# Kernel optimization log

Measured on AMD Instinct MI355X. Metric: run time of the kernel, lower is better.

The kernel has to match this reference:

```python
import jax, jax.numpy as jnp
import numpy as np

B, DIM, HEADS, HW = 32, 384, 8, 48
CH = DIM // HEADS  # 48 channels per head


def pool_matrix(H, s):
    # PyTorch AdaptiveAvgPool2d binning: start=floor(i*H/s), end=ceil((i+1)*H/s)
    P = np.zeros((s, H), np.float32)
    for i in range(s):
        a = (i * H) // s
        b = -((-(i + 1) * H) // s)
        P[i, a:b] = 1.0 / (b - a)
    return jnp.asarray(P)


def dwconv(x, w, b, p):
    # depthwise conv, NCHW, kernel [C,1,k,k], stride 1, symmetric pad p
    y = jax.lax.conv_general_dilated(
        x, w, (1, 1), [(p, p), (p, p)],
        dimension_numbers=('NCHW', 'OIHW', 'NCHW'),
        feature_group_count=x.shape[1])
    if b is not None:
        y = y + b[None, :, None, None]
    return y


def setup_inputs() -> dict:
    key = jax.random.key(0)
    ks = jax.random.split(key, 10)
    s = 0.02
    return {
        'x': jax.random.normal(ks[0], (B, DIM, HW, HW), jnp.float32),
        'ln_w': jnp.ones((DIM,), jnp.float32),
        'ln_b': jnp.zeros((DIM,), jnp.float32),
        'w_qkv': jax.random.normal(ks[1], (3 * DIM, DIM), jnp.float32) * s,
        'w_dw': jax.random.normal(ks[2], (3 * DIM, 1, 3, 3), jnp.float32) * s,
        'temperature': jnp.ones((HEADS, 1, 1), jnp.float32),
        'conv3_w': jax.random.normal(ks[3], (3 * CH, 1, 3, 3), jnp.float32) * s,
        'conv3_b': jnp.zeros((3 * CH,), jnp.float32),
        'conv5_w': jax.random.normal(ks[4], (3 * CH, 1, 5, 5), jnp.float32) * s,
        'conv5_b': jnp.zeros((3 * CH,), jnp.float32),
        'conv7_w': jax.random.normal(ks[5], (2 * CH, 1, 7, 7), jnp.float32) * s,
        'conv7_b': jnp.zeros((2 * CH,), jnp.float32),
        'w_proj': jax.random.normal(ks[6], (DIM, DIM), jnp.float32) * s,
    }


def reference(x, ln_w, ln_b, w_qkv, w_dw, temperature,
              conv3_w, conv3_b, conv5_w, conv5_b, conv7_w, conv7_b, w_proj):
    b, C, H, W = x.shape
    heads, Ch = HEADS, C // HEADS
    N = H * W
    # WithBias LayerNorm over channel dim (biased variance, eps 1e-5)
    mu = x.mean(axis=1, keepdims=True)
    var = ((x - mu) ** 2).mean(axis=1, keepdims=True)
    xn = (x - mu) / jnp.sqrt(var + 1e-5) * ln_w[None, :, None, None] + ln_b[None, :, None, None]
    # qkv: 1x1 conv then depthwise 3x3 (groups = 3*dim)
    qkv = jnp.einsum('bchw,oc->bohw', xn, w_qkv)
    qkv = dwconv(qkv, w_dw, None, 1)
    q, k, v = jnp.split(qkv, 3, axis=1)
    q = q.reshape(b, heads, Ch, N)
    k = k.reshape(b, heads, Ch, N)
    v = v.reshape(b, heads, Ch, N)
    # L2-normalize along token dim (F.normalize eps=1e-12)
    qn = q / jnp.maximum(jnp.linalg.norm(q, axis=-1, keepdims=True), 1e-12)
    kn = k / jnp.maximum(jnp.linalg.norm(k, axis=-1, keepdims=True), 1e-12)
    # channel attention [b,h,Ch,Ch]
    attn = jax.nn.relu(jnp.einsum('bhcn,bhdn->bhcd', qn, kn) * temperature[None])
    # ---- FilterModule (crpe) ----
    v_img = v.reshape(b, heads * Ch, H, W)
    # low-pass: 4 equal channel chunks, adaptive avg pool to (1,3,5,7), bilinear up
    chunk = (heads * Ch) // 4
    lp_parts = []
    for idx, sz in enumerate((1, 3, 5, 7)):
        part = v_img[:, idx * chunk:(idx + 1) * chunk]
        Pr = pool_matrix(H, sz)
        Pc = pool_matrix(W, sz)
        pooled = jnp.einsum('ph,bchw,qw->bcpq', Pr, part, Pc)
        lp_parts.append(jax.image.resize(pooled, (b, chunk, H, W), method='linear'))
    LP = jax.nn.relu(jnp.concatenate(lp_parts, axis=1))
    # high-pass: grouped depthwise convs on [3Ch, 3Ch, 2Ch] channel splits
    s0, s1 = 3 * Ch, 3 * Ch
    HP = jnp.concatenate([
        dwconv(v_img[:, :s0], conv3_w, conv3_b, 1),
        dwconv(v_img[:, s0:s0 + s1], conv5_w, conv5_b, 2),
        dwconv(v_img[:, s0 + s1:], conv7_w, conv7_b, 3),
    ], axis=1)
    HP = HP.reshape(b, heads, Ch, N)
    LPf = LP.reshape(b, heads, Ch, N)
    crpe = qn * HP + LPf
    # ---- output ----
    out = jnp.einsum('bhcd,bhdn->bhcn', attn, v)
    out = (Ch ** -0.5) * out + crpe
    out = out.reshape(b, C, H, W)
    out = jnp.einsum('bchw,oc->bohw', out, w_proj)
    return out
```

## Files before the change

### kernel.cpp

```cpp
#include <hip/hip_runtime.h>

typedef unsigned short u16;
typedef short sh4 __attribute__((ext_vector_type(4)));
typedef short short8 __attribute__((ext_vector_type(8)));
typedef u16 ush8 __attribute__((ext_vector_type(8)));
typedef __bf16 bf16x8 __attribute__((ext_vector_type(8)));
typedef float f32x4 __attribute__((ext_vector_type(4)));

#define NB 32
#define CDIM 384
#define NSP 2304
#define QCH 1152

__device__ __forceinline__ float b2f(u16 u) {
    union { unsigned i; float f; } v; v.i = ((unsigned)u) << 16; return v.f;
}
__device__ __forceinline__ u16 f2b(float f) {
    union { float f; unsigned i; } v; v.f = f;
    unsigned r = v.i + 0x7FFFu + ((v.i >> 16) & 1u);
    return (u16)(r >> 16);
}
__device__ __forceinline__ void gload16(const u16* g, u16* l) {
    __builtin_amdgcn_global_load_lds((const __attribute__((address_space(1))) unsigned int*)(g),
                                     (__attribute__((address_space(3))) unsigned int*)(l), 16, 0, 0);
}

__global__ __launch_bounds__(256) void k_prep(const float* __restrict__ wqkv,
                                              const float* __restrict__ wproj,
                                              u16* __restrict__ wqkv_bf,
                                              u16* __restrict__ wproj_bf) {
    int i = blockIdx.x * 256 + threadIdx.x;
    if (i < QCH * CDIM) wqkv_bf[i] = f2b(wqkv[i]);
    if (i < CDIM * CDIM) wproj_bf[i] = f2b(wproj[i]);
}

__global__ __launch_bounds__(256) void k_ln(const float* __restrict__ x,
                                            const float* __restrict__ lnw,
                                            const float* __restrict__ lnb,
                                            u16* __restrict__ xnt) {
    __shared__ float s_sum[4][64], s_sq[4][64], s_mu[64], s_rs[64];
    __shared__ u16 s_tile[64][392];
    int b = blockIdx.y, n0 = blockIdx.x * 64;
    int tid = threadIdx.x, c4 = tid >> 6, nl = tid & 63;
    int cbase = c4 * 96;
    const float* xb = x + (size_t)b * CDIM * NSP + (size_t)cbase * NSP + n0 + nl;
    float v[96];
    float sum = 0.f, sq = 0.f;
#pragma unroll
    for (int j = 0; j < 96; j++) {
        v[j] = xb[(size_t)j * NSP];
        sum += v[j]; sq += v[j] * v[j];
    }
    s_sum[c4][nl] = sum; s_sq[c4][nl] = sq;
    __syncthreads();
    if (tid < 64) {
        float s = s_sum[0][tid] + s_sum[1][tid] + s_sum[2][tid] + s_sum[3][tid];
        float q = s_sq[0][tid] + s_sq[1][tid] + s_sq[2][tid] + s_sq[3][tid];
        float mu = s * (1.f / CDIM);
        float var = q * (1.f / CDIM) - mu * mu;
        s_mu[tid] = mu; s_rs[tid] = rsqrtf(var + 1e-5f);
    }
    __syncthreads();
    float mu = s_mu[nl], rs = s_rs[nl];
#pragma unroll
    for (int j = 0; j < 96; j++) {
        int c = cbase + j;
        s_tile[nl][c] = f2b((v[j] - mu) * rs * lnw[c] + lnb[c]);
    }
    __syncthreads();
    u16* o = xnt + ((size_t)b * NSP + n0) * CDIM;
    for (int i = tid; i < 64 * 48; i += 256) {
        int row = i / 48, c8 = i % 48;
        *(short8*)(o + row * CDIM + c8 * 8) = *(const short8*)(&s_tile[row][c8 * 8]);
    }
}

__global__ __launch_bounds__(256) void k_gemm(const u16* __restrict__ A,
                                              const u16* __restrict__ Bt,
                                              void* __restrict__ Cmat, int M, int f32out) {
    __shared__ __align__(16) u16 As[128 * 64];
    __shared__ __align__(16) u16 Bs[128 * 64];
    int tid = threadIdx.x;
    int bxn = blockIdx.x, bym = blockIdx.y, bz = blockIdx.z;
    int wave = tid >> 6, lane = tid & 63, wr = wave >> 1, wc = wave & 1;
    int lr = lane & 15, lk = lane >> 4;
    f32x4 acc[4][4];
#pragma unroll
    for (int m = 0; m < 4; m++)
#pragma unroll
        for (int n = 0; n < 4; n++) acc[m][n] = (f32x4){0.f, 0.f, 0.f, 0.f};
    int coloff = ((lane & 7) ^ (lane >> 3)) * 8;
    int rsub = lane >> 3;
    const u16* Ag = A + (size_t)(bym * 128 + wave * 32 + rsub) * 384 + coloff;
    const u16* Bg = Bt + ((size_t)bz * NSP + bxn * 128 + wave * 32 + rsub) * 384 + coloff;
    u16* Al = As + (wave * 4) * 512;
    u16* Bl = Bs + (wave * 4) * 512;
    for (int k0 = 0; k0 < 384; k0 += 64) {
#pragma unroll
        for (int i = 0; i < 4; i++) {
            gload16(Ag + (size_t)(i * 8) * 384 + k0, Al + i * 512);
            gload16(Bg + (size_t)(i * 8) * 384 + k0, Bl + i * 512);
        }
        __syncthreads();
        short8 bfr[4][2];
#pragma unroll
        for (int n = 0; n < 4; n++) {
            int row = wc * 64 + n * 16 + lr;
#pragma unroll
            for (int h = 0; h < 2; h++)
                bfr[n][h] = *(const short8*)(Bs + row * 64 + ((h * 4 + lk) ^ (lr & 7)) * 8);
        }
#pragma unroll
        for (int m = 0; m < 4; m++) {
            int row = wr * 64 + m * 16 + lr;
            short8 a0 = *(const short8*)(As + row * 64 + ((lk) ^ (lr & 7)) * 8);
            short8 a1 = *(const short8*)(As + row * 64 + ((4 + lk) ^ (lr & 7)) * 8);
#pragma unroll
            for (int n = 0; n < 4; n++) {
                acc[m][n] = __builtin_amdgcn_mfma_f32_16x16x32_bf16(
                    __builtin_bit_cast(bf16x8, a0), __builtin_bit_cast(bf16x8, bfr[n][0]),
                    acc[m][n], 0, 0, 0);
                acc[m][n] = __builtin_amdgcn_mfma_f32_16x16x32_bf16(
                    __builtin_bit_cast(bf16x8, a1), __builtin_bit_cast(bf16x8, bfr[n][1]),
                    acc[m][n], 0, 0, 0);
            }
        }
        __syncthreads();
    }
#pragma unroll
    for (int m = 0; m < 4; m++)
#pragma unroll
        for (int n = 0; n < 4; n++) {
            int row = bym * 128 + wr * 64 + m * 16 + lk * 4;
            int col = bxn * 128 + wc * 64 + n * 16 + lr;
            if (f32out) {
                float* cp = (float*)Cmat + ((size_t)bz * M + row) * NSP + col;
#pragma unroll
                for (int r = 0; r < 4; r++) cp[(size_t)r * NSP] = acc[m][n][r];
            } else {
                u16* cp = (u16*)Cmat + ((size_t)bz * M + row) * NSP + col;
#pragma unroll
                for (int r = 0; r < 4; r++) cp[(size_t)r * NSP] = f2b(acc[m][n][r]);
            }
        }
}

__global__ __launch_bounds__(192) void k_dw3(u16* __restrict__ qkv,
                                             const float* __restrict__ wdw,
                                             float* __restrict__ sumsq) {
    __shared__ u16 s_in[4 * 2304];
    __shared__ float s_part[192];
    int bx = blockIdx.x, b = blockIdx.y, tid = threadIdx.x;
    u16* gbase = qkv + ((size_t)b * QCH + bx * 4) * NSP;
#pragma unroll
    for (int i = 0; i < 6; i++) {
        int c = tid + i * 192;
        *(ush8*)(&s_in[c * 8]) = *(const ush8*)(gbase + c * 8);
    }
    int p = tid / 48, y = tid % 48;
    int ch = bx * 4 + p;
    float w[9];
#pragma unroll
    for (int i = 0; i < 9; i++) w[i] = wdw[ch * 9 + i];
    __syncthreads();
    const u16* L = &s_in[p * 2304];
    ush8 r0[6], r1[6], r2[6];
#pragma unroll
    for (int o = 0; o < 6; o++) {
        r1[o] = *(const ush8*)(L + y * 48 + o * 8);
        if (y > 0)  r0[o] = *(const ush8*)(L + (y - 1) * 48 + o * 8); else r0[o] = 0;
        if (y < 47) r2[o] = *(const ush8*)(L + (y + 1) * 48 + o * 8); else r2[o] = 0;
    }
    float ss = 0.f;
    short8 outv[6];
#pragma unroll
    for (int g = 0; g < 6; g++) {
        float a0[10], a1[10], a2[10];
#pragma unroll
        for (int j = 0; j < 10; j++) {
            int xi = g * 8 - 1 + j;
            if (xi < 0 || xi >= 48) { a0[j] = 0.f; a1[j] = 0.f; a2[j] = 0.f; }
            else {
                a0[j] = b2f(r0[xi >> 3][xi & 7]);
                a1[j] = b2f(r1[xi >> 3][xi & 7]);
                a2[j] = b2f(r2[xi >> 3][xi & 7]);
            }
        }
        union { u16 u[8]; short8 v; } pk;
#pragma unroll
        for (int x = 0; x < 8; x++) {
            float o = a0[x] * w[0] + a0[x + 1] * w[1] + a0[x + 2] * w[2]
                    + a1[x] * w[3] + a1[x + 1] * w[4] + a1[x + 2] * w[5]
                    + a2[x] * w[6] + a2[x + 1] * w[7] + a2[x + 2] * w[8];
            ss += o * o;
            pk.u[x] = f2b(o);
        }
        outv[g] = pk.v;
    }
    s_part[tid] = ss;
    __syncthreads();
#pragma unroll
    for (int g = 0; g < 6; g++)
        *(short8*)(&s_in[p * 2304 + y * 48 + g * 8]) = outv[g];
    __syncthreads();
#pragma unroll
    for (int i = 0; i < 6; i++) {
        int c = tid + i * 192;
        *(ush8*)(gbase + c * 8) = *(const ush8*)(&s_in[c * 8]);
    }
    if (bx < 192 && tid < 4) {
        float s = 0.f;
        for (int i = 0; i < 48; i++) s += s_part[tid * 48 + i];
        sumsq[b * 768 + bx * 4 + tid] = s;
    }
}

__global__ __launch_bounds__(512) void k_attn(const u16* __restrict__ qkv,
                                              const float* __restrict__ sumsq,
                                              const float* __restrict__ temp,
                                              u16* __restrict__ attn) {
    __shared__ float s_part[8][48 * 48];
    int h = blockIdx.x, b = blockIdx.y, tid = threadIdx.x;
    int wave = tid >> 6, lane = tid & 63;
    int lr = lane & 15, lk = lane >> 4;
    const u16* qp = qkv + ((size_t)b * QCH + h * 48) * NSP;
    const u16* kp = qkv + ((size_t)b * QCH + 384 + h * 48) * NSP;
    f32x4 acc[3][3];
#pragma unroll
    for (int m = 0; m < 3; m++)
#pragma unroll
        for (int n = 0; n < 3; n++) acc[m][n] = (f32x4){0.f, 0.f, 0.f, 0.f};
    int k0 = wave * 288 + lk * 8;
    short8 af[3], bf[3], afn[3], bfn[3];
#pragma unroll
    for (int m = 0; m < 3; m++) {
        af[m] = *(const short8*)(qp + (size_t)(m * 16 + lr) * NSP + k0);
        bf[m] = *(const short8*)(kp + (size_t)(m * 16 + lr) * NSP + k0);
    }
    for (int s = 0; s < 9; s++) {
        if (s < 8) {
#pragma unroll
            for (int m = 0; m < 3; m++) {
                afn[m] = *(const short8*)(qp + (size_t)(m * 16 + lr) * NSP + k0 + 32 * (s + 1));
                bfn[m] = *(const short8*)(kp + (size_t)(m * 16 + lr) * NSP + k0 + 32 * (s + 1));
            }
        }
#pragma unroll
        for (int m = 0; m < 3; m++)
#pragma unroll
            for (int n = 0; n < 3; n++)
                acc[m][n] = __builtin_amdgcn_mfma_f32_16x16x32_bf16(
                    __builtin_bit_cast(bf16x8, af[m]), __builtin_bit_cast(bf16x8, bf[n]),
                    acc[m][n], 0, 0, 0);
#pragma unroll
        for (int m = 0; m < 3; m++) { af[m] = afn[m]; bf[m] = bfn[m]; }
    }
#pragma unroll
    for (int m = 0; m < 3; m++)
#pragma unroll
        for (int n = 0; n < 3; n++)
#pragma unroll
            for (int r = 0; r < 4; r++)
                s_part[wave][(m * 16 + lk * 4 + r) * 48 + n * 16 + lr] = acc[m][n][r];
    __syncthreads();
    float th = temp[h];
    const float* sqv = sumsq + b * 768 + h * 48;
    const float* skv = sumsq + b * 768 + 384 + h * 48;
    u16* ap = attn + ((size_t)(b * 8 + h)) * NSP;
    for (int f = tid; f < 2304; f += 512) {
        int c = f / 48, d = f % 48;
        float v = 0.f;
#pragma unroll
        for (int wv = 0; wv < 8; wv++) v += s_part[wv][f];
        float rq = 1.f / fmaxf(sqrtf(sqv[c]), 1e-12f);
        float rk = 1.f / fmaxf(sqrtf(skv[d]), 1e-12f);
        v *= th * rq * rk;
        ap[f] = f2b(fmaxf(v, 0.f));
    }
}

template<int KS, int CH0, int NCH>
__device__ __forceinline__ void hp_body(int g, const u16* __restrict__ qkv,
                                        const float* __restrict__ wk,
                                        const float* __restrict__ bk,
                                        u16* __restrict__ hp) {
    constexpr int PAD = KS / 2;
    constexpr int NIN = 8 + 2 * PAD;
    int t = g * 256 + threadIdx.x;
    int y = t % 48;
    int rem = t / 48;
    int chl = rem % NCH;
    int b = rem / NCH;
    int ch = CH0 + chl;
    const u16* src = qkv + ((size_t)b * QCH + 768 + ch) * NSP;
    float bias = bk[chl];
    float acc[48];
#pragma unroll
    for (int i = 0; i < 48; i++) acc[i] = bias;
    for (int dy = 0; dy < KS; dy++) {
        int yy = y - PAD + dy;
        if (yy < 0 || yy >= 48) continue;
        ush8 r[6];
#pragma unroll
        for (int o = 0; o < 6; o++) r[o] = *(const ush8*)(src + yy * 48 + o * 8);
        float wr[KS];
#pragma unroll
        for (int dx = 0; dx < KS; dx++) wr[dx] = wk[chl * KS * KS + dy * KS + dx];
#pragma unroll
        for (int g2 = 0; g2 < 6; g2++) {
            float a[NIN];
#pragma unroll
            for (int j = 0; j < NIN; j++) {
                int xi = g2 * 8 - PAD + j;
                a[j] = (xi < 0 || xi >= 48) ? 0.f : b2f(r[xi >> 3][xi & 7]);
            }
#pragma unroll
            for (int x = 0; x < 8; x++) {
                float s = 0.f;
#pragma unroll
                for (int dx = 0; dx < KS; dx++) s += a[x + dx] * wr[dx];
                acc[g2 * 8 + x] += s;
            }
        }
    }
    u16* dst = hp + ((size_t)b * CDIM + ch) * NSP + y * 48;
#pragma unroll
    for (int g2 = 0; g2 < 6; g2++) {
        union { u16 u[8]; short8 v; } pk;
#pragma unroll
        for (int x = 0; x < 8; x++) pk.u[x] = f2b(acc[g2 * 8 + x]);
        *(short8*)(dst + g2 * 8) = pk.v;
    }
}

__global__ __launch_bounds__(256) void k_hp(const u16* __restrict__ qkv,
                                            const float* __restrict__ w3, const float* __restrict__ b3,
                                            const float* __restrict__ w5, const float* __restrict__ b5,
                                            const float* __restrict__ w7, const float* __restrict__ b7,
                                            u16* __restrict__ hp) {
    int g = blockIdx.x;
    if (g < 864)       hp_body<3, 0, 144>(g, qkv, w3, b3, hp);
    else if (g < 1728) hp_body<5, 144, 144>(g - 864, qkv, w5, b5, hp);
    else               hp_body<7, 288, 96>(g - 1728, qkv, w7, b7, hp);
}

__global__ __launch_bounds__(64) void k_pool(const u16* __restrict__ qkv,
                                             float* __restrict__ pooled) {
    int c = blockIdx.x, b = blockIdx.y, tid = threadIdx.x;
    int s = 2 * (c / 96) + 1;
    __shared__ u16 s_p[2304];
    __shared__ float rp[48][7];
    const u16* src = qkv + ((size_t)b * QCH + 768 + c) * NSP;
    for (int f = tid; f < 288; f += 64)
        *(ush8*)(&s_p[f * 8]) = *(const ush8*)(src + f * 8);
    __syncthreads();
    if (tid < 48) {
        for (int q = 0; q < s; q++) {
            int a = q * 48 / s, e = ((q + 1) * 48 + s - 1) / s;
            float sum = 0.f;
            for (int xx = a; xx < e; xx++) sum += b2f(s_p[tid * 48 + xx]);
            rp[tid][q] = sum / (float)(e - a);
        }
    }
    __syncthreads();
    if (tid < s * s) {
        int p = tid / s, q = tid % s;
        int a = p * 48 / s, e = ((p + 1) * 48 + s - 1) / s;
        float sum = 0.f;
        for (int r = a; r < e; r++) sum += rp[r][q];
        pooled[((size_t)b * CDIM + c) * 49 + tid] = sum / (float)(e - a);
    }
}

__global__ __launch_bounds__(256) void k_out(const u16* __restrict__ qkv,
                                             const u16* __restrict__ attn,
                                             const float* __restrict__ sumsq,
                                             const u16* __restrict__ hp,
                                             const float* __restrict__ pooled,
                                             u16* __restrict__ tmpt) {
    int ncg = blockIdx.x, h = blockIdx.y, b = blockIdx.z, tid = threadIdx.x;
    __shared__ __align__(16) u16 s_at[48 * 72];
    __shared__ __align__(16) u16 s_vt[64 * 72];
    __shared__ float s_pool[48 * 49];
    __shared__ float s_rq[48];
    int s = 2 * (h / 2) + 1, ss2 = s * s;
    if (tid < 96) {
        int c = tid >> 1, col8 = 48 + (tid & 1) * 8;
        *(ush8*)(&s_at[c * 72 + col8]) = (ush8)0;
    }
    if (tid < 128) {
        int nn = tid >> 1, col8 = 48 + (tid & 1) * 8;
        *(ush8*)(&s_vt[nn * 72 + col8]) = (ush8)0;
    }
    const u16* ag = attn + ((size_t)(b * 8 + h)) * NSP;
    for (int f = tid; f < 288; f += 256) {
        int c = f / 6, j = f % 6;
        *(ush8*)(&s_at[c * 72 + j * 8]) = *(const ush8*)(ag + c * 48 + j * 8);
    }
    const float* psrc = pooled + ((size_t)b * CDIM + h * 48) * 49;
    for (int f = tid; f < 48 * ss2; f += 256) {
        int c = f / ss2, idx = f - c * ss2;
        s_pool[c * 49 + idx] = psrc[c * 49 + idx];
    }
    if (tid < 48) s_rq[tid] = 1.f / fmaxf(sqrtf(sumsq[b * 768 + h * 48 + tid]), 1e-12f);

    int wave = tid >> 6, lane = tid & 63, lr = lane & 15, lk = lane >> 4;
    const u16* vbase = qkv + ((size_t)b * QCH + 768 + h * 48) * NSP;
    const u16* qbase = qkv + ((size_t)b * QCH + h * 48) * NSP;
    const u16* hbase = hp + ((size_t)b * CDIM + h * 48) * NSP;
    const float inv = 0.14433756729740643f;
    short8 afr[3][2];

    for (int it = 0; it < 9; it++) {
        int n0 = (ncg * 9 + it) * 64;
        for (int f = tid; f < 3072; f += 256) {
            int d = f >> 6, nn = f & 63;
            s_vt[nn * 72 + d] = vbase[(size_t)d * NSP + n0 + nn];
        }
        __syncthreads();
        if (it == 0) {
#pragma unroll
            for (int m = 0; m < 3; m++)
#pragma unroll
                for (int ks = 0; ks < 2; ks++)
                    afr[m][ks] = *(const short8*)(&s_at[(m * 16 + lr) * 72 + ks * 32 + lk * 8]);
        }
        short8 b0 = *(const short8*)(&s_vt[(wave * 16 + lr) * 72 + lk * 8]);
        short8 b1 = *(const short8*)(&s_vt[(wave * 16 + lr) * 72 + 32 + lk * 8]);
        f32x4 acc[3];
#pragma unroll
        for (int m = 0; m < 3; m++) {
            acc[m] = (f32x4){0.f, 0.f, 0.f, 0.f};
            acc[m] = __builtin_amdgcn_mfma_f32_16x16x32_bf16(
                __builtin_bit_cast(bf16x8, afr[m][0]), __builtin_bit_cast(bf16x8, b0),
                acc[m], 0, 0, 0);
            acc[m] = __builtin_amdgcn_mfma_f32_16x16x32_bf16(
                __builtin_bit_cast(bf16x8, afr[m][1]), __builtin_bit_cast(bf16x8, b1),
                acc[m], 0, 0, 0);
        }
        int nl_e = wave * 16 + lr;
        int n = n0 + nl_e;
        int y = n / 48, xx = n % 48;
        int iy0 = 0, iy1 = 0, ix0 = 0, ix1 = 0;
        float fy = 0.f, fx = 0.f;
        if (s > 1) {
            float syf = (y + 0.5f) * s * (1.f / 48.f) - 0.5f;
            iy0 = (int)floorf(syf); fy = syf - (float)iy0;
            iy1 = min(iy0 + 1, s - 1); iy0 = max(iy0, 0);
            float sxf = (xx + 0.5f) * s * (1.f / 48.f) - 0.5f;
            ix0 = (int)floorf(sxf); fx = sxf - (float)ix0;
            ix1 = min(ix0 + 1, s - 1); ix0 = max(ix0, 0);
        }
        const u16* qp = qbase + n;
        const u16* hq = hbase + n;
        u16* tp = tmpt + ((size_t)b * NSP + n) * CDIM + h * 48;
#pragma unroll
        for (int m = 0; m < 3; m++) {
            int cb = m * 16 + lk * 4;
            union { u16 u[4]; sh4 v; } pk;
#pragma unroll
            for (int r = 0; r < 4; r++) {
                int ch = cb + r;
                float qv = b2f(qp[(size_t)ch * NSP]);
                float hv = b2f(hq[(size_t)ch * NSP]);
                const float* P = &s_pool[ch * 49];
                float lp;
                if (s == 1) lp = P[0];
                else lp = (1.f - fy) * ((1.f - fx) * P[iy0 * s + ix0] + fx * P[iy0 * s + ix1])
                        + fy * ((1.f - fx) * P[iy1 * s + ix0] + fx * P[iy1 * s + ix1]);
                lp = fmaxf(lp, 0.f);
                pk.u[r] = f2b(inv * acc[m][r] + qv * s_rq[ch] * hv + lp);
            }
            *(sh4*)(tp + cb) = pk.v;
        }
        __syncthreads();
    }
}

extern "C" void kernel_launch(void* const* d_in, const int* in_sizes, int n_in,
                              void* d_out, int out_size, void* d_ws, size_t ws_size,
                              hipStream_t stream) {
    const float* x    = (const float*)d_in[0];
    const float* lnw  = (const float*)d_in[1];
    const float* lnb  = (const float*)d_in[2];
    const float* wqkv = (const float*)d_in[3];
    const float* wdw  = (const float*)d_in[4];
    const float* temp = (const float*)d_in[5];
    const float* w3   = (const float*)d_in[6];
    const float* b3   = (const float*)d_in[7];
    const float* w5   = (const float*)d_in[8];
    const float* b5   = (const float*)d_in[9];
    const float* w7   = (const float*)d_in[10];
    const float* b7   = (const float*)d_in[11];
    const float* wproj= (const float*)d_in[12];
    float* out = (float*)d_out;

    char* w = (char*)d_ws;
    const size_t SZ_XNT = (size_t)NB * NSP * CDIM * 2;
    const size_t SZ_QKV = (size_t)NB * QCH * NSP * 2;
    u16* xnt      = (u16*)w;
    u16* qkvb     = (u16*)(w + SZ_XNT);
    u16* hpb      = (u16*)(w + SZ_XNT + SZ_QKV);
    char* tail    = w + SZ_XNT + SZ_QKV + (size_t)NB * CDIM * NSP * 2;
    float* sumsq  = (float*)tail;
    u16*  attnb   = (u16*)(sumsq + NB * 768);
    float* pooled = (float*)(attnb + (size_t)NB * 8 * NSP);
    u16* wqkv_bf  = (u16*)(pooled + (size_t)NB * CDIM * 49);
    u16* wproj_bf = wqkv_bf + (size_t)QCH * CDIM;
    u16* tmpt = xnt;

    k_prep <<<dim3((QCH * CDIM + 255) / 256), 256, 0, stream>>>(wqkv, wproj, wqkv_bf, wproj_bf);
    k_ln   <<<dim3(36, NB), 256, 0, stream>>>(x, lnw, lnb, xnt);
    k_gemm <<<dim3(18, 9, NB), 256, 0, stream>>>(wqkv_bf, xnt, qkvb, QCH, 0);
    k_dw3  <<<dim3(288, NB), 192, 0, stream>>>(qkvb, wdw, sumsq);
    k_attn <<<dim3(8, NB), 512, 0, stream>>>(qkvb, sumsq, temp, attnb);
    k_hp   <<<dim3(2304), 256, 0, stream>>>(qkvb, w3, b3, w5, b5, w7, b7, hpb);
    k_pool <<<dim3(CDIM, NB), 64, 0, stream>>>(qkvb, pooled);
    k_out  <<<dim3(4, 8, NB), 256, 0, stream>>>(qkvb, attnb, sumsq, hpb, pooled, tmpt);
    k_gemm <<<dim3(18, 3, NB), 256, 0, stream>>>(wproj_bf, tmpt, out, CDIM, 1);
}
```

Measured before the change: 425.0 us.

## Stage GEMM epilogue through LDS for coalesced stores and swizzle block order

The GEMM epilogue now writes accumulators into shared memory and then issues 16-byte vectorized, row-contiguous global stores instead of scattered 2/4-byte strided stores, for both the bf16 and fp32 outputs. It also remaps the flat block index so groups of 8 consecutive blocks share an M tile across neighbouring N panels, aiming for better L2 reuse. The shared buffers are merged into one array to hold the output tile, which adds extra syncs and LDS traffic in the epilogue. The remap hardcodes 18 N panels and assumes the grid factors cleanly.

```diff
diff --git a/kernel.cpp b/kernel.cpp
--- a/kernel.cpp
+++ b/kernel.cpp
@@ -78,10 +78,16 @@
 __global__ __launch_bounds__(256) void k_gemm(const u16* __restrict__ A,
                                               const u16* __restrict__ Bt,
                                               void* __restrict__ Cmat, int M, int f32out) {
-    __shared__ __align__(16) u16 As[128 * 64];
-    __shared__ __align__(16) u16 Bs[128 * 64];
+    __shared__ __align__(16) u16 S[128 * 128];
+    u16* As = S;
+    u16* Bs = S + 8192;
     int tid = threadIdx.x;
-    int bxn = blockIdx.x, bym = blockIdx.y, bz = blockIdx.z;
+    int nym = gridDim.y;
+    int flat = blockIdx.x + gridDim.x * (blockIdx.y + nym * blockIdx.z);
+    int p = flat & 7, q = flat >> 3;
+    int bym = q % nym;
+    int panel = (q / nym) * 8 + p;
+    int bxn = panel % 18, bz = panel / 18;
     int wave = tid >> 6, lane = tid & 63, wr = wave >> 1, wc = wave & 1;
     int lr = lane & 15, lk = lane >> 4;
     f32x4 acc[4][4];
@@ -127,22 +133,48 @@
         }
         __syncthreads();
     }
-#pragma unroll
-    for (int m = 0; m < 4; m++)
-#pragma unroll
-        for (int n = 0; n < 4; n++) {
-            int row = bym * 128 + wr * 64 + m * 16 + lk * 4;
-            int col = bxn * 128 + wc * 64 + n * 16 + lr;
-            if (f32out) {
-                float* cp = (float*)Cmat + ((size_t)bz * M + row) * NSP + col;
-#pragma unroll
-                for (int r = 0; r < 4; r++) cp[(size_t)r * NSP] = acc[m][n][r];
-            } else {
-                u16* cp = (u16*)Cmat + ((size_t)bz * M + row) * NSP + col;
-#pragma unroll
-                for (int r = 0; r < 4; r++) cp[(size_t)r * NSP] = f2b(acc[m][n][r]);
-            }
-        }
+    if (!f32out) {
+#pragma unroll
+        for (int m = 0; m < 4; m++)
+#pragma unroll
+            for (int n = 0; n < 4; n++)
+#pragma unroll
+                for (int r = 0; r < 4; r++)
+                    S[(wr * 64 + m * 16 + lk * 4 + r) * 128 + wc * 64 + n * 16 + lr] =
+                        f2b(acc[m][n][r]);
+        __syncthreads();
+        u16* Cg = (u16*)Cmat + ((size_t)bz * M + bym * 128) * NSP + bxn * 128;
+#pragma unroll
+        for (int i = 0; i < 8; i++) {
+            int f = tid + i * 256;
+            int row = f >> 4, c8 = f & 15;
+            *(short8*)(Cg + (size_t)row * NSP + c8 * 8) = *(const short8*)(&S[row * 128 + c8 * 8]);
+        }
+    } else {
+        float* Sf = (float*)S;
+        float* Cg = (float*)Cmat + ((size_t)bz * M + bym * 128) * NSP + bxn * 128;
+#pragma unroll
+        for (int half = 0; half < 2; half++) {
+            if (wr == half) {
+#pragma unroll
+                for (int m = 0; m < 4; m++)
+#pragma unroll
+                    for (int n = 0; n < 4; n++)
+#pragma unroll
+                        for (int r = 0; r < 4; r++)
+                            Sf[(m * 16 + lk * 4 + r) * 128 + wc * 64 + n * 16 + lr] = acc[m][n][r];
+            }
+            __syncthreads();
+#pragma unroll
+            for (int i = 0; i < 8; i++) {
+                int f = tid + i * 256;
+                int row = f >> 5, c4 = f & 31;
+                *(f32x4*)(Cg + (size_t)(half * 64 + row) * NSP + c4 * 4) =
+                    *(const f32x4*)(&Sf[row * 128 + c4 * 4]);
+            }
+            __syncthreads();
+        }
+    }
 }
 
 __global__ __launch_bounds__(192) void k_dw3(u16* __restrict__ qkv,
```

After: 404.0 us, median of 2. 1.05x faster.
